# Kernel tuning notes

Hardware: AMD Instinct MI355X
Metric: run time of the kernel (lower is better)

Reference implementation:

```python
import jax, jax.numpy as jnp
import numpy as np

B, T, D, H, L = 64, 512, 256, 512, 4


def setup_inputs() -> dict:
    key = jax.random.key(0)
    ks = jax.random.split(key, 1 + 2 * L)
    inp = {"x": jax.random.normal(ks[0], (B, T, D), dtype=jnp.float32)}
    s = 0.05
    for l in range(L):
        in_dim = D if l == 0 else H
        inp[f"W{l}"] = jax.random.normal(ks[1 + 2 * l], (4 * H, in_dim), dtype=jnp.float32) * s
        inp[f"U{l}"] = jax.random.normal(ks[2 + 2 * l], (4 * H, H), dtype=jnp.float32) * s
        inp[f"bw{l}"] = jnp.zeros((4 * H,), dtype=jnp.float32)
        inp[f"bu{l}"] = jnp.zeros((4 * H,), dtype=jnp.float32)
    return inp


def _lstm_forward(x, params):
    # x: [B, T, D]; params: list of (W [4H,in], U [4H,H], bw [4H], bu [4H])
    Bq = x.shape[0]
    h0 = [jnp.zeros((Bq, H), x.dtype) for _ in range(L)]
    c0 = [jnp.zeros((Bq, H), x.dtype) for _ in range(L)]

    def step(carry, x_t):
        hs, cs = carry
        new_h, new_c = [], []
        inp = x_t  # [B, in]
        for (W, U, bw, bu), h_i, c_i in zip(params, hs, cs):
            z = inp @ W.T + bw + h_i @ U.T + bu  # [B, 4H]
            f, i, o, g = jnp.split(z, 4, axis=-1)  # gate order f,i,o,g
            f = jax.nn.sigmoid(f)
            i = jax.nn.sigmoid(i)
            o = jax.nn.sigmoid(o)
            g = jnp.tanh(g)
            c_n = f * c_i + i * g
            h_n = o * jnp.tanh(c_n)
            new_h.append(h_n)
            new_c.append(c_n)
            inp = h_n
        return (new_h, new_c), inp

    (h_f, c_f), out = jax.lax.scan(step, (h0, c0), jnp.swapaxes(x, 0, 1))
    output = jnp.swapaxes(out, 0, 1)  # [B, T, H]
    return output, jnp.stack(h_f), jnp.stack(c_f)


def reference(x, W0, U0, bw0, bu0, W1, U1, bw1, bu1, W2, U2, bw2, bu2, W3, U3, bw3, bu3):
    params = [(W0, U0, bw0, bu0), (W1, U1, bw1, bu1), (W2, U2, bw2, bu2), (W3, U3, bw3, bu3)]
    return _lstm_forward(x, params)
```

## Files before the change

kernel.cpp:

```cpp
#include <hip/hip_runtime.h>

typedef __attribute__((ext_vector_type(8))) short bf16x8;
typedef __attribute__((ext_vector_type(4))) float f32x4;

#define WPL 32
#define NT 256
#define RING 8

__device__ __forceinline__ unsigned short f2bf(float f) {
  unsigned int u = __float_as_uint(f);
  u += 0x7FFFu + ((u >> 16) & 1u);
  return (unsigned short)(u >> 16);
}
__device__ __forceinline__ float sigmoid_fast(float x) {
  return __builtin_amdgcn_rcpf(1.0f + __builtin_amdgcn_exp2f(-1.4426950408889634f * x));
}
__device__ __forceinline__ float tanh_fast(float x) {
  return 1.0f - 2.0f * __builtin_amdgcn_rcpf(
                           1.0f + __builtin_amdgcn_exp2f(2.885390081777927f * x));
}
__device__ __forceinline__ void wait_vm0() {
  asm volatile("s_waitcnt vmcnt(0)" ::: "memory");
  __builtin_amdgcn_sched_barrier(0);
}
#define WAITVM(N)                                         \
  do {                                                    \
    asm volatile("s_waitcnt vmcnt(" #N ")" ::: "memory"); \
    __builtin_amdgcn_sched_barrier(0);                    \
  } while (0)

template <int MODE>
__device__ __forceinline__ void ldA(bf16x8& d, int voff, const unsigned short* base) {
  if constexpr (MODE == 0)
    asm volatile("global_load_dwordx4 %0, %1, %2"
                 : "=v"(d) : "v"(voff), "s"(base));
  else
    asm volatile("global_load_dwordx4 %0, %1, %2 sc0 sc1"
                 : "=v"(d) : "v"(voff), "s"(base));
}
__device__ __forceinline__ unsigned ld_flag(const unsigned* p) {
  unsigned v;
  asm volatile("global_load_dword %0, %1, off sc0 sc1\n\ts_waitcnt vmcnt(0)"
               : "=v"(v) : "v"(p) : "memory");
  return v;
}
__device__ __forceinline__ void st16_coh(void* p, f32x4 v) {
  asm volatile("global_store_dwordx4 %0, %1, off sc0 sc1" :: "v"(p), "v"(v) : "memory");
}
__device__ __forceinline__ void st4_coh(void* p, unsigned v) {
  asm volatile("global_store_dword %0, %1, off sc0 sc1" :: "v"(p), "v"(v) : "memory");
}


__global__ void cvt_x_kernel(const float* __restrict__ x,
                             unsigned short* __restrict__ xf) {
  int tid = blockIdx.x * 256 + threadIdx.x;
  int t     = tid >> 11;
  int inner = tid & 2047;
  int lane  = inner & 63;
  int bt    = (inner >> 6) & 3;
  int c     = inner >> 8;
  int b = bt * 16 + (lane & 15);
  int d = c * 32 + (lane >> 4) * 8;
  const float* s = x + ((size_t)b * 512 + t) * 256 + d;
  f32x4 v0 = *(const f32x4*)s;
  f32x4 v1 = *(const f32x4*)(s + 4);
  bf16x8 o;
  o[0] = (short)f2bf(v0[0]); o[1] = (short)f2bf(v0[1]);
  o[2] = (short)f2bf(v0[2]); o[3] = (short)f2bf(v0[3]);
  o[4] = (short)f2bf(v1[0]); o[5] = (short)f2bf(v1[1]);
  o[6] = (short)f2bf(v1[2]); o[7] = (short)f2bf(v1[3]);
  *(bf16x8*)(xf + (size_t)t * 16384 + (size_t)inner * 8) = o;
}

__global__ void cvt_w_kernel(const float* __restrict__ W,
                             const float* __restrict__ U,
                             unsigned short* __restrict__ dst,
                             int C2, int split) {
  int tid = blockIdx.x * 256 + threadIdx.x;
  int lane = tid & 63;
  int c    = (tid >> 6) % C2;
  int rest = tid / (64 * C2);
  int g = rest & 3;
  int w = rest >> 2;
  int row = g * 512 + w * 16 + (lane & 15);
  int k   = c * 32 + (lane >> 4) * 8;
  const float* s = (k < split) ? (W + (size_t)row * split + k)
                               : (U + (size_t)row * 512 + (k - split));
  f32x4 v0 = *(const f32x4*)s;
  f32x4 v1 = *(const f32x4*)(s + 4);
  bf16x8 o;
  o[0] = (short)f2bf(v0[0]); o[1] = (short)f2bf(v0[1]);
  o[2] = (short)f2bf(v0[2]); o[3] = (short)f2bf(v0[3]);
  o[4] = (short)f2bf(v1[0]); o[5] = (short)f2bf(v1[1]);
  o[6] = (short)f2bf(v1[2]); o[7] = (short)f2bf(v1[3]);
  *(bf16x8*)(dst + (size_t)tid * 8) = o;
}

__global__ void bias_kernel(const float* __restrict__ bw,
                            const float* __restrict__ bu,
                            float* __restrict__ dst) {
  int i = blockIdx.x * 256 + threadIdx.x;
  dst[i] = bw[i] + bu[i];
}

__global__ void zero_flags(unsigned int* __restrict__ p) {
  int i = blockIdx.x * 256 + threadIdx.x;
  p[i] = 0u;
}

template <int NC, int MODE>
__device__ __forceinline__ void gemm_part(const unsigned short* __restrict__ a,
                                          const char* bg0, const char* bg1,
                                          const char* bg2, const char* bg3,
                                          int voffA, f32x4 acc[4]) {
  constexpr int NP = NC / 4;
  bf16x8 av[3][4];
  bf16x8 bb[2][4][4];
  const char* bgp[4] = {bg0, bg1, bg2, bg3};

  auto issueA_phase = [&](int q) {
#pragma unroll
    for (int i = 0; i < 4; ++i)
      ldA<MODE>(av[q % 3][i], voffA + (4 * q + i) * 4096, a);
  };
  auto loadB_phase = [&](int q) {
#pragma unroll
    for (int i = 0; i < 4; ++i)
#pragma unroll
      for (int g = 0; g < 4; ++g)
        bb[q & 1][i][g] = *(const bf16x8*)(bgp[g] + (4 * q + i) * 1024);
  };

#pragma unroll
  for (int q = 0; q < 3; ++q)
    if (q < NP) issueA_phase(q);
  loadB_phase(0);

#pragma unroll
  for (int ph = 0; ph < NP; ++ph) {
    if (ph + 1 < NP) loadB_phase(ph + 1);
    if (ph < NP - 2) {
      WAITVM(8);
    } else if (ph == NP - 2) {
      WAITVM(4);
    } else {
      WAITVM(0);
    }
#pragma unroll
    for (int i = 0; i < 4; ++i)
#pragma unroll
      for (int g = 0; g < 4; ++g)
        acc[g] = __builtin_amdgcn_mfma_f32_16x16x32_bf16(av[ph % 3][i],
                                                         bb[ph & 1][i][g],
                                                         acc[g], 0, 0, 0);
    if (ph + 3 < NP) issueA_phase(ph + 3);
  }
}

__global__ void __launch_bounds__(NT, 1)
lstm_main(const unsigned short* __restrict__ xfrag,
          const unsigned short* __restrict__ wf0,
          const unsigned short* __restrict__ wf1,
          const unsigned short* __restrict__ wf2,
          const unsigned short* __restrict__ wf3,
          const float* __restrict__ bias,
          unsigned short* __restrict__ hbuf,
          unsigned int* __restrict__ flags,
          float* __restrict__ out) {
  extern __shared__ char smem[];

  const int bid   = blockIdx.x;
  const int layer = bid >> 5;
  const int w     = bid & 31;
  const int tid   = threadIdx.x;
  const int lane  = tid & 63;
  const int vm    = tid >> 6;
  const int l15   = lane & 15;
  const int lhi   = lane >> 4;
  const int hcol  = w * 16 + l15;
  const int C2r   = (layer == 0) ? 24 : 32;
  const int C1w   = (layer == 0) ? 8 : 16;
  const int HOFF  = 4 * C2r * 64 * 16;

  const unsigned short* wfl =
      (layer == 0) ? wf0 : (layer == 1) ? wf1 : (layer == 2) ? wf2 : wf3;
  const unsigned short* wsl = wfl + (size_t)w * (4 * C2r * 64 * 8);

  for (int i = tid; i < 4 * C2r * 64; i += NT)
    *(f32x4*)(smem + (size_t)i * 16) = *(const f32x4*)(wsl + (size_t)i * 8);
  __syncthreads();

  const char* bgW[4];
  const char* bgU[4];
#pragma unroll
  for (int g = 0; g < 4; ++g) {
    bgW[g] = smem + ((size_t)g * C2r * 64 + lane) * 16;
    bgU[g] = bgW[g] + (size_t)C1w * 1024;
  }

  float bv[4];
#pragma unroll
  for (int g = 0; g < 4; ++g) bv[g] = bias[layer * 2048 + g * 512 + hcol];

  float creg[4];
#pragma unroll
  for (int r = 0; r < 4; ++r) creg[r] = 0.f;

  const int voffA = lane * 16 + vm * 1024;
  const int base_w = (w >> 1) * 2048 + (w & 1) * 256;

  const unsigned short* hprev =
      (layer == 0) ? nullptr : (hbuf + (size_t)(layer - 1) * RING * 32768);
  const unsigned short* hself = hbuf + (size_t)layer * RING * 32768;

  const int sb_bt = tid >> 5;
  const int sb_q  = (tid >> 4) & 1;
  const int sb_bl = tid & 15;
  const int slot_off = base_w + sb_bt * 512 + sb_q * 128 + sb_bl * 8;

  for (int t = 0; t < 512; ++t) {
    if (vm == 0) {
      const unsigned* fp = flags;
      unsigned need = 0;
      if (lane < 32 && layer > 0) {
        fp = flags + ((layer - 1) * 32 + lane) * 16;
        need = (unsigned)(t + 1);
      }
      while (true) {
        unsigned v = need ? ld_flag(fp) : 0u;
        if (__ballot(need && v < need) == 0) break;
        __builtin_amdgcn_s_sleep(1);
      }
    } else if (vm == 1) {
      const unsigned* fp = flags;
      unsigned need = 0;
      if (lane < 32 && layer < 3 && t >= RING) {
        fp = flags + ((layer + 1) * 32 + lane) * 16;
        need = (unsigned)(t - RING + 1);
      }
      while (true) {
        unsigned v = need ? ld_flag(fp) : 0u;
        if (__ballot(need && v < need) == 0) break;
        __builtin_amdgcn_s_sleep(1);
      }
    }
    __syncthreads();
    wait_vm0();

    f32x4 acc[4];
    const f32x4 z4 = {0.f, 0.f, 0.f, 0.f};
#pragma unroll
    for (int g = 0; g < 4; ++g) acc[g] = z4;

    if (layer == 0)
      gemm_part<8, 0>(xfrag + (size_t)t * 16384,
                      bgW[0], bgW[1], bgW[2], bgW[3], voffA, acc);
    else
      gemm_part<16, 2>(hprev + (size_t)(t & (RING - 1)) * 32768,
                       bgW[0], bgW[1], bgW[2], bgW[3], voffA, acc);

    if (t > 0) {
      if (vm == 0) {
        const unsigned* fp = flags;
        unsigned need = 0;
        if (lane < 32) {
          fp = flags + (layer * 32 + lane) * 16;
          need = (unsigned)t;
        }
        while (true) {
          unsigned v = need ? ld_flag(fp) : 0u;
          if (__ballot(need && v < need) == 0) break;
          __builtin_amdgcn_s_sleep(1);
        }
      }
      __syncthreads();

      gemm_part<16, 2>(hself + (size_t)((t - 1) & (RING - 1)) * 32768,
                       bgU[0], bgU[1], bgU[2], bgU[3], voffA, acc);
    }

    float hreg[4], cnreg[4];
#pragma unroll
    for (int r = 0; r < 4; ++r) {
      float fg = sigmoid_fast(acc[0][r] + bv[0]);
      float ig = sigmoid_fast(acc[1][r] + bv[1]);
      float og = sigmoid_fast(acc[2][r] + bv[2]);
      float gg = tanh_fast(acc[3][r] + bv[3]);
      float cn = fg * creg[r] + ig * gg;
      creg[r] = cn;
      cnreg[r] = cn;
      float h = og * tanh_fast(cn);
      hreg[r] = h;
      *(unsigned short*)(smem + HOFF + (vm * 16 + lhi * 4 + r) * 32 + l15 * 2) =
          f2bf(h);
    }
    __syncthreads();

    if (tid < 128) {
      f32x4 hv = *(const f32x4*)(smem + HOFF + (sb_bt * 16 + sb_bl) * 32 + sb_q * 16);
      unsigned short* dst = hbuf +
          ((size_t)layer * RING + (t & (RING - 1))) * 32768 + slot_off;
      st16_coh(dst, hv);
      wait_vm0();
    }
    __syncthreads();
    if (tid == 0)
      st4_coh(flags + (layer * 32 + w) * 16, (unsigned)(t + 1));

    if (layer == 3) {
#pragma unroll
      for (int r = 0; r < 4; ++r) {
        int bidx = vm * 16 + lhi * 4 + r;
        out[(size_t)bidx * 262144 + (size_t)t * 512 + hcol] = hreg[r];
      }
    }
    if (t == 511) {
#pragma unroll
      for (int r = 0; r < 4; ++r) {
        int bidx = vm * 16 + lhi * 4 + r;
        out[16777216 + ((size_t)layer * 64 + bidx) * 512 + hcol] = hreg[r];
        out[16777216 + 131072 + ((size_t)layer * 64 + bidx) * 512 + hcol] = cnreg[r];
      }
    }
  }
}

extern "C" void kernel_launch(void* const* d_in, const int* in_sizes, int n_in,
                              void* d_out, int out_size, void* d_ws, size_t ws_size,
                              hipStream_t stream) {
  const float* x = (const float*)d_in[0];
  const float *W[4], *U[4], *bw[4], *bu[4];
  for (int l = 0; l < 4; ++l) {
    W[l]  = (const float*)d_in[1 + 4 * l];
    U[l]  = (const float*)d_in[2 + 4 * l];
    bw[l] = (const float*)d_in[3 + 4 * l];
    bu[l] = (const float*)d_in[4 + 4 * l];
  }

  char* ws = (char*)d_ws;
  unsigned short* xfrag = (unsigned short*)(ws + 0);
  unsigned short* wfr0  = (unsigned short*)(ws + 16777216);
  unsigned short* wfr1  = (unsigned short*)(ws + 19922944);
  unsigned short* wfr2  = (unsigned short*)(ws + 24117248);
  unsigned short* wfr3  = (unsigned short*)(ws + 28311552);
  float*          biasp = (float*)(ws + 32505856);
  unsigned short* hbuf  = (unsigned short*)(ws + 32538624);
  unsigned int*   flags = (unsigned int*)(ws + 34635776);
  float* out = (float*)d_out;

  cvt_x_kernel<<<4096, 256, 0, stream>>>(x, xfrag);
  cvt_w_kernel<<<768, 256, 0, stream>>>(W[0], U[0], wfr0, 24, 256);
  cvt_w_kernel<<<1024, 256, 0, stream>>>(W[1], U[1], wfr1, 32, 512);
  cvt_w_kernel<<<1024, 256, 0, stream>>>(W[2], U[2], wfr2, 32, 512);
  cvt_w_kernel<<<1024, 256, 0, stream>>>(W[3], U[3], wfr3, 32, 512);
  bias_kernel<<<8, 256, 0, stream>>>(bw[0], bu[0], biasp + 0 * 2048);
  bias_kernel<<<8, 256, 0, stream>>>(bw[1], bu[1], biasp + 1 * 2048);
  bias_kernel<<<8, 256, 0, stream>>>(bw[2], bu[2], biasp + 2 * 2048);
  bias_kernel<<<8, 256, 0, stream>>>(bw[3], bu[3], biasp + 3 * 2048);
  zero_flags<<<8, 256, 0, stream>>>(flags);

  hipFuncSetAttribute((const void*)lstm_main,
                      hipFuncAttributeMaxDynamicSharedMemorySize, 135168);
  lstm_main<<<dim3(4 * WPL), dim3(NT), 135168, stream>>>(
      xfrag, wfr0, wfr1, wfr2, wfr3, biasp, hbuf, flags, out);
}
```

Baseline: 1.876 ms.

## Merge W and U GEMMs into one pipelined pass with a single per-step barrier

Each timestep now makes one pipelined pass over a concatenated K range that covers the input part and the recurrent part, instead of two separate pipelined GEMM calls. All flag waits (upstream layer, own layer's previous step, downstream ring space) move into one combined spin-wait and barrier at the end of the step, replacing two barriers per step. This removes one pipeline drain/refill and one __syncthreads per step on the serial recurrent critical path. In exchange, the input-projection GEMM can no longer start before the own-layer h from the previous step is ready.

```diff
diff --git a/kernel.cpp b/kernel.cpp
--- a/kernel.cpp
+++ b/kernel.cpp
@@ -109,20 +109,26 @@
   p[i] = 0u;
 }
 
-template <int NC, int MODE>
-__device__ __forceinline__ void gemm_part(const unsigned short* __restrict__ a,
-                                          const char* bg0, const char* bg1,
-                                          const char* bg2, const char* bg3,
-                                          int voffA, f32x4 acc[4]) {
-  constexpr int NP = NC / 4;
+template <int C1, int C2, int M1, int M2>
+__device__ __forceinline__ void gemm_run(const unsigned short* __restrict__ a1,
+                                         const unsigned short* __restrict__ a2,
+                                         const char* bg0, const char* bg1,
+                                         const char* bg2, const char* bg3,
+                                         int voffA, f32x4 acc[4]) {
+  constexpr int NP = C2 / 4;
   bf16x8 av[3][4];
   bf16x8 bb[2][4][4];
   const char* bgp[4] = {bg0, bg1, bg2, bg3};
 
+  auto issueA_iter = [&](int cc, int s3, int i) {
+    if (cc < C1)
+      ldA<M1>(av[s3][i], voffA + cc * 4096, a1);
+    else
+      ldA<M2>(av[s3][i], voffA + (cc - C1) * 4096, a2);
+  };
   auto issueA_phase = [&](int q) {
 #pragma unroll
-    for (int i = 0; i < 4; ++i)
-      ldA<MODE>(av[q % 3][i], voffA + (4 * q + i) * 4096, a);
+    for (int i = 0; i < 4; ++i) issueA_iter(4 * q + i, q % 3, i);
   };
   auto loadB_phase = [&](int q) {
 #pragma unroll
@@ -180,7 +186,6 @@
   const int lhi   = lane >> 4;
   const int hcol  = w * 16 + l15;
   const int C2r   = (layer == 0) ? 24 : 32;
-  const int C1w   = (layer == 0) ? 8 : 16;
   const int HOFF  = 4 * C2r * 64 * 16;
 
   const unsigned short* wfl =
@@ -191,13 +196,9 @@
     *(f32x4*)(smem + (size_t)i * 16) = *(const f32x4*)(wsl + (size_t)i * 8);
   __syncthreads();
 
-  const char* bgW[4];
-  const char* bgU[4];
-#pragma unroll
-  for (int g = 0; g < 4; ++g) {
-    bgW[g] = smem + ((size_t)g * C2r * 64 + lane) * 16;
-    bgU[g] = bgW[g] + (size_t)C1w * 1024;
-  }
+  const char* bg[4];
+#pragma unroll
+  for (int g = 0; g < 4; ++g) bg[g] = smem + ((size_t)g * C2r * 64 + lane) * 16;
 
   float bv[4];
 #pragma unroll
@@ -219,65 +220,44 @@
   const int sb_bl = tid & 15;
   const int slot_off = base_w + sb_bt * 512 + sb_q * 128 + sb_bl * 8;
 
+  if (layer > 0 && vm == 0) {
+    const unsigned* fp = flags;
+    unsigned need = 0;
+    if (lane < 32) {
+      fp = flags + ((layer - 1) * 32 + lane) * 16;
+      need = 1u;
+    }
+    while (true) {
+      unsigned v = need ? ld_flag(fp) : 0u;
+      if (__ballot(need && v < need) == 0) break;
+      __builtin_amdgcn_s_sleep(1);
+    }
+  }
+  __syncthreads();
+  wait_vm0();
+
   for (int t = 0; t < 512; ++t) {
-    if (vm == 0) {
-      const unsigned* fp = flags;
-      unsigned need = 0;
-      if (lane < 32 && layer > 0) {
-        fp = flags + ((layer - 1) * 32 + lane) * 16;
-        need = (unsigned)(t + 1);
-      }
-      while (true) {
-        unsigned v = need ? ld_flag(fp) : 0u;
-        if (__ballot(need && v < need) == 0) break;
-        __builtin_amdgcn_s_sleep(1);
-      }
-    } else if (vm == 1) {
-      const unsigned* fp = flags;
-      unsigned need = 0;
-      if (lane < 32 && layer < 3 && t >= RING) {
-        fp = flags + ((layer + 1) * 32 + lane) * 16;
-        need = (unsigned)(t - RING + 1);
-      }
-      while (true) {
-        unsigned v = need ? ld_flag(fp) : 0u;
-        if (__ballot(need && v < need) == 0) break;
-        __builtin_amdgcn_s_sleep(1);
-      }
-    }
-    __syncthreads();
-    wait_vm0();
+    const unsigned short* aW =
+        (layer == 0) ? (xfrag + (size_t)t * 16384)
+                     : (hprev + (size_t)(t & (RING - 1)) * 32768);
+    const unsigned short* aU =
+        hself + (size_t)((t - 1) & (RING - 1)) * 32768;
 
     f32x4 acc[4];
     const f32x4 z4 = {0.f, 0.f, 0.f, 0.f};
 #pragma unroll
     for (int g = 0; g < 4; ++g) acc[g] = z4;
 
-    if (layer == 0)
-      gemm_part<8, 0>(xfrag + (size_t)t * 16384,
-                      bgW[0], bgW[1], bgW[2], bgW[3], voffA, acc);
-    else
-      gemm_part<16, 2>(hprev + (size_t)(t & (RING - 1)) * 32768,
-                       bgW[0], bgW[1], bgW[2], bgW[3], voffA, acc);
-
-    if (t > 0) {
-      if (vm == 0) {
-        const unsigned* fp = flags;
-        unsigned need = 0;
-        if (lane < 32) {
-          fp = flags + (layer * 32 + lane) * 16;
-          need = (unsigned)t;
-        }
-        while (true) {
-          unsigned v = need ? ld_flag(fp) : 0u;
-          if (__ballot(need && v < need) == 0) break;
-          __builtin_amdgcn_s_sleep(1);
-        }
-      }
-      __syncthreads();
-
-      gemm_part<16, 2>(hself + (size_t)((t - 1) & (RING - 1)) * 32768,
-                       bgU[0], bgU[1], bgU[2], bgU[3], voffA, acc);
+    if (t == 0) {
+      if (layer == 0)
+        gemm_run<8, 8, 0, 0>(aW, aW, bg[0], bg[1], bg[2], bg[3], voffA, acc);
+      else
+        gemm_run<16, 16, 2, 2>(aW, aW, bg[0], bg[1], bg[2], bg[3], voffA, acc);
+    } else {
+      if (layer == 0)
+        gemm_run<8, 24, 0, 2>(aW, aU, bg[0], bg[1], bg[2], bg[3], voffA, acc);
+      else
+        gemm_run<16, 32, 2, 2>(aW, aU, bg[0], bg[1], bg[2], bg[3], voffA, acc);
     }
 
     float hreg[4], cnreg[4];
@@ -323,6 +303,41 @@
         out[16777216 + 131072 + ((size_t)layer * 64 + bidx) * 512 + hcol] = cnreg[r];
       }
     }
+
+    if (t < 511) {
+      if (vm == 0) {
+        const unsigned* fp = flags;
+        unsigned need = 0;
+        if (lane < 32) {
+          if (layer > 0) {
+            fp = flags + ((layer - 1) * 32 + lane) * 16;
+            need = (unsigned)(t + 2);
+          }
+        } else {
+          fp = flags + (layer * 32 + (lane - 32)) * 16;
+          need = (unsigned)(t + 1);
+        }
+        while (true) {
+          unsigned v = need ? ld_flag(fp) : 0u;
+          if (__ballot(need && v < need) == 0) break;
+          __builtin_amdgcn_s_sleep(1);
+        }
+      } else if (vm == 1) {
+        const unsigned* fp = flags;
+        unsigned need = 0;
+        if (lane < 32 && layer < 3 && (t + 1) >= RING) {
+          fp = flags + ((layer + 1) * 32 + lane) * 16;
+          need = (unsigned)(t + 2 - RING);
+        }
+        while (true) {
+          unsigned v = need ? ld_flag(fp) : 0u;
+          if (__ballot(need && v < need) == 0) break;
+          __builtin_amdgcn_s_sleep(1);
+        }
+      }
+      __syncthreads();
+      wait_vm0();
+    }
   }
 }
 
```

Result: no change. 1.891 ms (+0.8%).

## Prefetch next step's input activations and overlap flag waits across waves

Applied to the files above, without the earlier changes.

Replaces the phased gemm helper with register-resident A fragments: the input-side (x or previous-layer h) operands for step t+1 are loaded at the end of step t, and the recurrent h operands are issued at the start of the step and consumed in four chunks with staged vmcnt waits. The cross-layer flag polls move into waves 2 and 3 during the h-store phase, so they run alongside the store instead of before the GEMM. Every wave now spins on its own layer's flags before the next step, which drops one block barrier. This shortens the serial critical path per timestep at the cost of more VGPRs and more redundant polling traffic.

```diff
diff --git a/kernel.cpp b/kernel.cpp
--- a/kernel.cpp
+++ b/kernel.cpp
@@ -109,55 +109,6 @@
   p[i] = 0u;
 }
 
-template <int NC, int MODE>
-__device__ __forceinline__ void gemm_part(const unsigned short* __restrict__ a,
-                                          const char* bg0, const char* bg1,
-                                          const char* bg2, const char* bg3,
-                                          int voffA, f32x4 acc[4]) {
-  constexpr int NP = NC / 4;
-  bf16x8 av[3][4];
-  bf16x8 bb[2][4][4];
-  const char* bgp[4] = {bg0, bg1, bg2, bg3};
-
-  auto issueA_phase = [&](int q) {
-#pragma unroll
-    for (int i = 0; i < 4; ++i)
-      ldA<MODE>(av[q % 3][i], voffA + (4 * q + i) * 4096, a);
-  };
-  auto loadB_phase = [&](int q) {
-#pragma unroll
-    for (int i = 0; i < 4; ++i)
-#pragma unroll
-      for (int g = 0; g < 4; ++g)
-        bb[q & 1][i][g] = *(const bf16x8*)(bgp[g] + (4 * q + i) * 1024);
-  };
-
-#pragma unroll
-  for (int q = 0; q < 3; ++q)
-    if (q < NP) issueA_phase(q);
-  loadB_phase(0);
-
-#pragma unroll
-  for (int ph = 0; ph < NP; ++ph) {
-    if (ph + 1 < NP) loadB_phase(ph + 1);
-    if (ph < NP - 2) {
-      WAITVM(8);
-    } else if (ph == NP - 2) {
-      WAITVM(4);
-    } else {
-      WAITVM(0);
-    }
-#pragma unroll
-    for (int i = 0; i < 4; ++i)
-#pragma unroll
-      for (int g = 0; g < 4; ++g)
-        acc[g] = __builtin_amdgcn_mfma_f32_16x16x32_bf16(av[ph % 3][i],
-                                                         bb[ph & 1][i][g],
-                                                         acc[g], 0, 0, 0);
-    if (ph + 3 < NP) issueA_phase(ph + 3);
-  }
-}
-
 __global__ void __launch_bounds__(NT, 1)
 lstm_main(const unsigned short* __restrict__ xfrag,
           const unsigned short* __restrict__ wf0,
@@ -175,12 +126,12 @@
   const int w     = bid & 31;
   const int tid   = threadIdx.x;
   const int lane  = tid & 63;
-  const int vm    = tid >> 6;
+  const int wv    = tid >> 6;
+  const int vm    = wv;
   const int l15   = lane & 15;
   const int lhi   = lane >> 4;
   const int hcol  = w * 16 + l15;
   const int C2r   = (layer == 0) ? 24 : 32;
-  const int C1w   = (layer == 0) ? 8 : 16;
   const int HOFF  = 4 * C2r * 64 * 16;
 
   const unsigned short* wfl =
@@ -191,13 +142,9 @@
     *(f32x4*)(smem + (size_t)i * 16) = *(const f32x4*)(wsl + (size_t)i * 8);
   __syncthreads();
 
-  const char* bgW[4];
-  const char* bgU[4];
-#pragma unroll
-  for (int g = 0; g < 4; ++g) {
-    bgW[g] = smem + ((size_t)g * C2r * 64 + lane) * 16;
-    bgU[g] = bgW[g] + (size_t)C1w * 1024;
-  }
+  const char* bg[4];
+#pragma unroll
+  for (int g = 0; g < 4; ++g) bg[g] = smem + ((size_t)g * C2r * 64 + lane) * 16;
 
   float bv[4];
 #pragma unroll
@@ -219,65 +166,83 @@
   const int sb_bl = tid & 15;
   const int slot_off = base_w + sb_bt * 512 + sb_q * 128 + sb_bl * 8;
 
+  bf16x8 aw[16];
+  if (layer > 0) {
+    while (true) {
+      const unsigned* fp = (lane < 32) ? (flags + ((layer - 1) * 32 + lane) * 16)
+                                       : flags;
+      unsigned need = (lane < 32) ? 1u : 0u;
+      unsigned v = ld_flag(fp);
+      if (__ballot(need && v < need) == 0) break;
+      __builtin_amdgcn_s_sleep(1);
+    }
+#pragma unroll
+    for (int c = 0; c < 16; ++c) ldA<2>(aw[c], voffA + c * 4096, hprev);
+  } else {
+#pragma unroll
+    for (int c = 0; c < 8; ++c) ldA<0>(aw[c], voffA + c * 4096, xfrag);
+  }
+  wait_vm0();
+
   for (int t = 0; t < 512; ++t) {
-    if (vm == 0) {
-      const unsigned* fp = flags;
-      unsigned need = 0;
-      if (lane < 32 && layer > 0) {
-        fp = flags + ((layer - 1) * 32 + lane) * 16;
-        need = (unsigned)(t + 1);
-      }
-      while (true) {
-        unsigned v = need ? ld_flag(fp) : 0u;
-        if (__ballot(need && v < need) == 0) break;
-        __builtin_amdgcn_s_sleep(1);
-      }
-    } else if (vm == 1) {
-      const unsigned* fp = flags;
-      unsigned need = 0;
-      if (lane < 32 && layer < 3 && t >= RING) {
-        fp = flags + ((layer + 1) * 32 + lane) * 16;
-        need = (unsigned)(t - RING + 1);
-      }
-      while (true) {
-        unsigned v = need ? ld_flag(fp) : 0u;
-        if (__ballot(need && v < need) == 0) break;
-        __builtin_amdgcn_s_sleep(1);
-      }
-    }
-    __syncthreads();
-    wait_vm0();
-
     f32x4 acc[4];
     const f32x4 z4 = {0.f, 0.f, 0.f, 0.f};
 #pragma unroll
     for (int g = 0; g < 4; ++g) acc[g] = z4;
 
-    if (layer == 0)
-      gemm_part<8, 0>(xfrag + (size_t)t * 16384,
-                      bgW[0], bgW[1], bgW[2], bgW[3], voffA, acc);
-    else
-      gemm_part<16, 2>(hprev + (size_t)(t & (RING - 1)) * 32768,
-                       bgW[0], bgW[1], bgW[2], bgW[3], voffA, acc);
-
+    bf16x8 av[16];
     if (t > 0) {
-      if (vm == 0) {
-        const unsigned* fp = flags;
-        unsigned need = 0;
-        if (lane < 32) {
-          fp = flags + (layer * 32 + lane) * 16;
-          need = (unsigned)t;
-        }
-        while (true) {
-          unsigned v = need ? ld_flag(fp) : 0u;
-          if (__ballot(need && v < need) == 0) break;
-          __builtin_amdgcn_s_sleep(1);
-        }
-      }
-      __syncthreads();
-
-      gemm_part<16, 2>(hself + (size_t)((t - 1) & (RING - 1)) * 32768,
-                       bgU[0], bgU[1], bgU[2], bgU[3], voffA, acc);
+      const unsigned short* aU = hself + (size_t)((t - 1) & (RING - 1)) * 32768;
+#pragma unroll
+      for (int c = 0; c < 16; ++c) ldA<2>(av[c], voffA + c * 4096, aU);
+    }
+
+    if (layer == 0) {
+#pragma unroll
+      for (int c = 0; c < 8; ++c)
+#pragma unroll
+        for (int g = 0; g < 4; ++g)
+          acc[g] = __builtin_amdgcn_mfma_f32_16x16x32_bf16(
+              aw[c], *(const bf16x8*)(bg[g] + c * 1024), acc[g], 0, 0, 0);
+    } else {
+#pragma unroll
+      for (int c = 0; c < 16; ++c)
+#pragma unroll
+        for (int g = 0; g < 4; ++g)
+          acc[g] = __builtin_amdgcn_mfma_f32_16x16x32_bf16(
+              aw[c], *(const bf16x8*)(bg[g] + c * 1024), acc[g], 0, 0, 0);
+    }
+
+    if (t > 0) {
+      const int c0 = (layer == 0) ? 8 : 16;
+      WAITVM(12);
+#pragma unroll
+      for (int c = 0; c < 4; ++c)
+#pragma unroll
+        for (int g = 0; g < 4; ++g)
+          acc[g] = __builtin_amdgcn_mfma_f32_16x16x32_bf16(
+              av[c], *(const bf16x8*)(bg[g] + (c0 + c) * 1024), acc[g], 0, 0, 0);
+      WAITVM(8);
+#pragma unroll
+      for (int c = 4; c < 8; ++c)
+#pragma unroll
+        for (int g = 0; g < 4; ++g)
+          acc[g] = __builtin_amdgcn_mfma_f32_16x16x32_bf16(
+              av[c], *(const bf16x8*)(bg[g] + (c0 + c) * 1024), acc[g], 0, 0, 0);
+      WAITVM(4);
+#pragma unroll
+      for (int c = 8; c < 12; ++c)
+#pragma unroll
+        for (int g = 0; g < 4; ++g)
+          acc[g] = __builtin_amdgcn_mfma_f32_16x16x32_bf16(
+              av[c], *(const bf16x8*)(bg[g] + (c0 + c) * 1024), acc[g], 0, 0, 0);
+      WAITVM(0);
+#pragma unroll
+      for (int c = 12; c < 16; ++c)
+#pragma unroll
+        for (int g = 0; g < 4; ++g)
+          acc[g] = __builtin_amdgcn_mfma_f32_16x16x32_bf16(
+              av[c], *(const bf16x8*)(bg[g] + (c0 + c) * 1024), acc[g], 0, 0, 0);
     }
 
     float hreg[4], cnreg[4];
@@ -297,12 +262,36 @@
     }
     __syncthreads();
 
-    if (tid < 128) {
+    if (wv < 2) {
       f32x4 hv = *(const f32x4*)(smem + HOFF + (sb_bt * 16 + sb_bl) * 32 + sb_q * 16);
       unsigned short* dst = hbuf +
           ((size_t)layer * RING + (t & (RING - 1))) * 32768 + slot_off;
       st16_coh(dst, hv);
       wait_vm0();
+    } else if (wv == 2) {
+      if (t < 511 && layer > 0) {
+        while (true) {
+          const unsigned* fp = (lane < 32)
+                                   ? (flags + ((layer - 1) * 32 + lane) * 16)
+                                   : flags;
+          unsigned need = (lane < 32) ? (unsigned)(t + 2) : 0u;
+          unsigned v = ld_flag(fp);
+          if (__ballot(need && v < need) == 0) break;
+          __builtin_amdgcn_s_sleep(1);
+        }
+      }
+    } else {
+      if (t < 511 && layer < 3 && (t + 1) >= RING) {
+        while (true) {
+          const unsigned* fp = (lane < 32)
+                                   ? (flags + ((layer + 1) * 32 + lane) * 16)
+                                   : flags;
+          unsigned need = (lane < 32) ? (unsigned)(t + 2 - RING) : 0u;
+          unsigned v = ld_flag(fp);
+          if (__ballot(need && v < need) == 0) break;
+          __builtin_amdgcn_s_sleep(1);
+        }
+      }
     }
     __syncthreads();
     if (tid == 0)
@@ -323,7 +312,29 @@
         out[16777216 + 131072 + ((size_t)layer * 64 + bidx) * 512 + hcol] = cnreg[r];
       }
     }
+
+    if (t < 511) {
+      if (layer == 0) {
+        const unsigned short* aWn = xfrag + (size_t)(t + 1) * 16384;
+#pragma unroll
+        for (int c = 0; c < 8; ++c) ldA<0>(aw[c], voffA + c * 4096, aWn);
+      } else {
+        const unsigned short* aWn =
+            hprev + (size_t)((t + 1) & (RING - 1)) * 32768;
+#pragma unroll
+        for (int c = 0; c < 16; ++c) ldA<2>(aw[c], voffA + c * 4096, aWn);
+      }
+      while (true) {
+        const unsigned* fp = (lane < 32) ? (flags + (layer * 32 + lane) * 16)
+                                         : flags;
+        unsigned need = (lane < 32) ? (unsigned)(t + 1) : 0u;
+        unsigned v = ld_flag(fp);
+        if (__ballot(need && v < need) == 0) break;
+        __builtin_amdgcn_s_sleep(1);
+      }
+    }
   }
+  wait_vm0();
 }
 
 extern "C" void kernel_launch(void* const* d_in, const int* in_sizes, int n_in,
```

Result: slower. 2.395 ms (+27.7%).
